# Kernel tuning notes

Measured on AMD Instinct MI355X. Metric: run time of the kernel, lower is better.

## Reference

```python
import jax, jax.numpy as jnp
import numpy as np

B, S, N = 8, 512, 2048   # batch, seq_len (=input_dim=output_dim), num_features (graph nodes)
HID = 512
K = 8                    # k_neighbors


def _construct_adj(x, k):
    """Faithful port of construct_graph: note the original normalizes the
    (1, N) mean-feature vector along dim=1 (whole-vector L2 norm), so the
    'similarity matrix' is actually the outer product v v^T / ||v||^2."""
    Bn, Sn, Nn = x.shape
    fv = x.mean(axis=1)                                  # (B, N)
    nf = fv / jnp.linalg.norm(fv, axis=1, keepdims=True)  # whole-row L2 normalize
    sim = nf[:, :, None] * nf[:, None, :]                # (B, N, N) outer product
    kk = min(k, Nn - 1)
    _, idx = jax.lax.top_k(sim, kk + 1)                  # (B, N, kk+1)
    idx = idx[..., 1:]                                   # drop the single largest (B, N, kk)
    b_ix = jnp.arange(Bn)[:, None, None]
    r_ix = jnp.arange(Nn)[None, :, None]
    adj = jnp.zeros((Bn, Nn, Nn), x.dtype).at[b_ix, r_ix, idx].set(1.0)
    adj = jnp.maximum(adj, jnp.swapaxes(adj, 1, 2))      # symmetrize (adj[idx, i] = 1)
    d = jnp.arange(Nn)
    adj = adj.at[:, d, d].set(1.0)                       # fill_diagonal_(1)
    return adj


def _gc(x, adj, W, b):
    """GraphConvLayer: degree-normalized adjacency bmm after linear."""
    deg = adj.sum(axis=2, keepdims=True)                 # (B, N, 1)
    deg = jnp.where(deg == 0, jnp.ones_like(deg), deg)
    h = x @ W.T + b                                      # (B, N, out)
    return jnp.einsum('bij,bjh->bih', adj / deg, h)


def setup_inputs() -> dict:
    key = jax.random.key(0)
    k0, k1, k2 = jax.random.split(key, 3)
    x = jax.random.normal(k0, (B, S, N), jnp.float32)
    W1 = jax.random.normal(k1, (HID, S), jnp.float32) * 0.02
    b1 = jnp.zeros((HID,), jnp.float32)
    W2 = jax.random.normal(k2, (S, HID), jnp.float32) * 0.02
    b2 = jnp.zeros((S,), jnp.float32)
    return {"x": x, "W1": W1, "b1": b1, "W2": W2, "b2": b2}


def reference(x, W1, b1, W2, b2):
    adj = _construct_adj(x, K)                           # (B, N, N)
    xr = jnp.swapaxes(x, 1, 2)                           # (B, N, S)
    h = jax.nn.relu(_gc(xr, adj, W1, b1))                # (B, N, HID); dropout is eval no-op
    h = _gc(h, adj, W2, b2)                              # (B, N, S)
    return jnp.swapaxes(h, 1, 2)                         # (B, S, N)
```

## Files before the change

kernel.cpp:

```cpp
#include <hip/hip_runtime.h>
#include <hip/hip_bf16.h>
#include <cstdint>

typedef unsigned short u16;
typedef __bf16 bf16x8 __attribute__((ext_vector_type(8)));
typedef float f32x4 __attribute__((ext_vector_type(4)));
typedef float f32x8 __attribute__((ext_vector_type(8)));
typedef unsigned short u16x4 __attribute__((ext_vector_type(4)));
typedef unsigned short u16x8 __attribute__((ext_vector_type(8)));

#define BB 8
#define SS 512
#define NN 2048
#define HH 512
#define MM (BB*NN)

__device__ inline u16 f2b(float f) {
  __hip_bfloat16 h = __float2bfloat16(f);
  return *reinterpret_cast<u16*>(&h);
}
__device__ inline float b2f(u16 u) {
  unsigned x = ((unsigned)u) << 16;
  return __uint_as_float(x);
}
__device__ inline f32x8 b2f8(u16x8 v) {
  f32x8 r;
  #pragma unroll
  for (int k = 0; k < 8; ++k) r[k] = b2f(v[k]);
  return r;
}

#define GLOAD16(g, l) __builtin_amdgcn_global_load_lds( \
    (const __attribute__((address_space(1))) void*)(g), \
    (__attribute__((address_space(3))) void*)(l), 16, 0, 0)

__device__ inline void remap_mn(int bid, int& m0, int& n0) {
  const int xcd = bid & 7, k = bid >> 3;
  m0 = (xcd * 16 + (k >> 2)) * 128;
  n0 = (k & 3) * 128;
}

__global__ __launch_bounds__(256) void k_prep(const float* __restrict__ x, u16* __restrict__ xr,
                       float* __restrict__ fvp,
                       const float* __restrict__ W1, const float* __restrict__ W2,
                       u16* __restrict__ w1b, u16* __restrict__ w2b,
                       float* __restrict__ xs ) {
  const int u = blockIdx.x;
  const int tid = threadIdx.x;
  if (u < 4096) {
    __shared__ float t[64][33];
    __shared__ float ps[8][32];
    const int tx = tid & 31, ty = tid >> 5;
    const int n0 = (u & 63) * 32, st = (u >> 6) & 7, b = u >> 9;
    const int s0 = st * 64;
    float acc = 0.f;
    #pragma unroll
    for (int i = ty; i < 64; i += 8) {
      float w = x[(size_t)b*SS*NN + (size_t)(s0+i)*NN + n0 + tx];
      t[i][tx] = w; acc += w;
    }
    ps[ty][tx] = acc;
    __syncthreads();
    if (ty == 0) {
      float s = 0.f;
      #pragma unroll
      for (int j = 0; j < 8; ++j) s += ps[j][tx];
      fvp[((size_t)(b*8 + st))*NN + n0 + tx] = s;
    }
    const int wtx = tid & 15, wty = tid >> 4;
    #pragma unroll
    for (int j = wty; j < 32; j += 16) {
      ushort4 o;
      o.x = f2b(t[wtx*4+0][j]); o.y = f2b(t[wtx*4+1][j]);
      o.z = f2b(t[wtx*4+2][j]); o.w = f2b(t[wtx*4+3][j]);
      *(ushort4*)(xr + ((size_t)b*NN + n0 + j)*SS + s0 + wtx*4) = o;
    }
    if (u < 96) {
      ((float4*)xs)[u*256 + tid] = make_float4(0.f, 0.f, 0.f, 0.f);
    }
  } else {
    const int b2v = u - 4096;
    const float* Wsrc = (b2v >= 256) ? W2 : W1;
    u16* wb = (b2v >= 256) ? w2b : w1b;
    const int off = (b2v & 255) * 1024;
    float4 v = ((const float4*)(Wsrc + off))[tid];
    ushort4 o; o.x = f2b(v.x); o.y = f2b(v.y); o.z = f2b(v.z); o.w = f2b(v.w);
    *(ushort4*)(wb + off + tid*4) = o;
  }
}

__global__ __launch_bounds__(256) void k_tops(const float* __restrict__ fvp, const u16* __restrict__ xr,
                       int* __restrict__ meta, int* __restrict__ rowfl, float* __restrict__ xs) {
  const int tid = threadIdx.x;
  if (blockIdx.x < BB) {
    const int b = blockIdx.x;
    __shared__ float v[NN];
    __shared__ unsigned long long wk[8];
    __shared__ unsigned long long winner[2];
    __shared__ int sel[18];
    __shared__ int scnt[12];
    __shared__ int ccnt[12];
    const int wv = tid >> 6, ln = tid & 63;

    float lv[8];
    {
      f32x4 a0 = {0,0,0,0}, a1 = {0,0,0,0};
      for (int sb_ = 0; sb_ < 8; ++sb_) {
        const f32x4* p = (const f32x4*)(fvp + ((size_t)(b*8 + sb_))*NN + tid*8);
        a0 += p[0]; a1 += p[1];
      }
      lv[0]=a0[0]; lv[1]=a0[1]; lv[2]=a0[2]; lv[3]=a0[3];
      lv[4]=a1[0]; lv[5]=a1[1]; lv[6]=a1[2]; lv[7]=a1[3];
    }
    #pragma unroll
    for (int j = 0; j < 8; ++j) v[tid*8+j] = lv[j];

    unsigned long long kD[8], kA[8];
    #pragma unroll
    for (int j = 0; j < 8; ++j) {
      unsigned u = __float_as_uint(lv[j]);
      u = (u & 0x80000000u) ? ~u : (u | 0x80000000u);
      unsigned idx = (unsigned)(tid*8 + j);
      kD[j] = ((unsigned long long)u << 32) | (0xFFFFFFFFu - idx);
      kA[j] = ((unsigned long long)(~u) << 32) | (0xFFFFFFFFu - idx);
    }
    unsigned mskD = 0, mskA = 0;
    for (int r = 0; r < 9; ++r) {
      unsigned long long bD = 0ull, bA = 0ull;
      #pragma unroll
      for (int j = 0; j < 8; ++j) {
        if (!((mskD >> j) & 1) && kD[j] > bD) bD = kD[j];
        if (!((mskA >> j) & 1) && kA[j] > bA) bA = kA[j];
      }
      #pragma unroll
      for (int o = 32; o > 0; o >>= 1) {
        unsigned long long oD = __shfl_xor(bD, o, 64);
        unsigned long long oA = __shfl_xor(bA, o, 64);
        if (oD > bD) bD = oD;
        if (oA > bA) bA = oA;
      }
      if (ln == 0) { wk[wv] = bD; wk[4+wv] = bA; }
      __syncthreads();
      if (tid == 0) {
        unsigned long long mD = wk[0], mA = wk[4];
        #pragma unroll
        for (int q = 1; q < 4; ++q) {
          if (wk[q] > mD) mD = wk[q];
          if (wk[4+q] > mA) mA = wk[4+q];
        }
        winner[0] = mD; winner[1] = mA;
        sel[r]   = (int)(0xFFFFFFFFu - (unsigned)mD);
        sel[9+r] = (int)(0xFFFFFFFFu - (unsigned)mA);
      }
      __syncthreads();
      unsigned iD = 0xFFFFFFFFu - (unsigned)winner[0];
      unsigned iA = 0xFFFFFFFFu - (unsigned)winner[1];
      if ((int)(iD >> 3) == tid) mskD |= 1u << (iD & 7);
      if ((int)(iA >> 3) == tid) mskA |= 1u << (iA & 7);
    }

    int cp = 0, cn = 0, cz = 0;
    #pragma unroll
    for (int j = 0; j < 8; ++j) { cp += (lv[j] > 0.f); cn += (lv[j] < 0.f); cz += (lv[j] == 0.f); }
    #pragma unroll
    for (int o = 32; o > 0; o >>= 1) { cp += __shfl_xor(cp, o, 64); cn += __shfl_xor(cn, o, 64); cz += __shfl_xor(cz, o, 64); }
    if (ln == 0) { ccnt[wv] = cp; ccnt[4+wv] = cn; ccnt[8+wv] = cz; }
    __syncthreads();
    if (tid == 0) {
      int CP = 0, CN = 0, CZ = 0;
      #pragma unroll
      for (int q = 0; q < 4; ++q) { CP += ccnt[q]; CN += ccnt[4+q]; CZ += ccnt[8+q]; }
      scnt[0] = CP; scnt[1] = CN; scnt[2] = CZ;
      for (int t2 = 3; t2 < 12; ++t2) scnt[t2] = 0;
      for (int r = 1; r < 9; ++r) {
        float wD = v[sel[r]];   scnt[3] += (wD > 0.f); scnt[4] += (wD < 0.f); scnt[5] += (wD == 0.f);
        float wA = v[sel[9+r]]; scnt[6] += (wA > 0.f); scnt[7] += (wA < 0.f); scnt[8] += (wA == 0.f);
        float wZ = v[r];        scnt[9] += (wZ > 0.f); scnt[10] += (wZ < 0.f); scnt[11] += (wZ == 0.f);
      }
    }
    __syncthreads();
    #pragma unroll
    for (int j = 0; j < 8; ++j) {
      const int i = tid*8 + j;
      float w = lv[j];
      int cls = (w > 0.f) ? 0 : ((w < 0.f) ? 1 : 2);
      int mD = 0, mA = 0;
      #pragma unroll
      for (int r = 1; r < 9; ++r) { mD |= (sel[r] == i); mA |= (sel[9+r] == i); }
      int mZ8 = (i >= 1 && i <= 8);
      rowfl[b*NN + i] = cls | (mD << 2) | (mA << 3) | (mZ8 << 4);
    }
    if (tid < 18) meta[b*32 + tid] = sel[tid];
    if (tid >= 18 && tid < 30) meta[b*32 + tid] = scnt[tid - 18];
    __syncthreads();
    #pragma unroll
    for (int half = 0; half < 2; ++half) {
      const int d = tid + half*256;
      float a[9];
      #pragma unroll
      for (int q = 0; q < 9; ++q) a[q] = 0.f;
      for (int r = 1; r < 9; ++r) {
        int iD = sel[r];   float wD = v[iD]; int cD = (wD>0.f)?0:((wD<0.f)?1:2);
        float vD = b2f(xr[((size_t)b*NN + iD)*512 + d]);
        int iA = sel[9+r]; float wA = v[iA]; int cA = (wA>0.f)?0:((wA<0.f)?1:2);
        float vA = b2f(xr[((size_t)b*NN + iA)*512 + d]);
        float wZ = v[r];   int cZ = (wZ>0.f)?0:((wZ<0.f)?1:2);
        float vZ = b2f(xr[((size_t)b*NN + r)*512 + d]);
        #pragma unroll
        for (int q = 0; q < 3; ++q) {
          a[q]   += (cD == q) ? vD : 0.f;
          a[3+q] += (cA == q) ? vA : 0.f;
          a[6+q] += (cZ == q) ? vZ : 0.f;
        }
      }
      #pragma unroll
      for (int q = 0; q < 9; ++q) xs[((size_t)b*12 + 3 + q)*512 + d] = a[q];
    }
  } else {
    const int u = blockIdx.x - 8, b = u >> 5, c = u & 31, n0 = c*64;
    __shared__ f32x8 red[12][64];
    __shared__ int scls[64];
    if (tid < 64) {
      float s = 0.f;
      for (int sb_ = 0; sb_ < 8; ++sb_) s += fvp[((size_t)(b*8 + sb_))*NN + n0 + tid];
      scls[tid] = (s > 0.f) ? 0 : ((s < 0.f) ? 1 : 2);
    }
    __syncthreads();
    const int fc = tid & 63, rg = tid >> 6;
    f32x8 sp = {0,0,0,0,0,0,0,0}, sn = sp, sz = sp;
    for (int it = 0; it < 16; ++it) {
      const int nr = rg + it*4;
      const int cls = scls[nr];
      f32x8 hf = b2f8(*(const u16x8*)(xr + ((size_t)b*NN + n0 + nr)*512 + fc*8));
      if (cls == 0) sp += hf; else if (cls == 1) sn += hf; else sz += hf;
    }
    red[0*4+rg][fc] = sp; red[1*4+rg][fc] = sn; red[2*4+rg][fc] = sz;
    __syncthreads();
    if (rg == 0) {
      sp = red[0][fc] + red[1][fc] + red[2][fc] + red[3][fc];
      sn = red[4][fc] + red[5][fc] + red[6][fc] + red[7][fc];
      sz = red[8][fc] + red[9][fc] + red[10][fc] + red[11][fc];
      #pragma unroll
      for (int j = 0; j < 8; ++j) {
        atomicAdd(&xs[((size_t)b*12 + 0)*512 + fc*8 + j], sp[j]);
        atomicAdd(&xs[((size_t)b*12 + 1)*512 + fc*8 + j], sn[j]);
        atomicAdd(&xs[((size_t)b*12 + 2)*512 + fc*8 + j], sz[j]);
      }
    }
  }
}

template<int MODE>
__global__ __launch_bounds__(256, 2) void k_gemmf(const u16* __restrict__ A, const u16* __restrict__ Bw,
                       const float* __restrict__ bias, const float* __restrict__ sums,
                       const int* __restrict__ meta, const int* __restrict__ rowfl,
                       void* __restrict__ outp, float* __restrict__ osum) {
  __shared__ __align__(16) char SM[49472];
  u16* As  = (u16*)SM;
  u16* Bs  = (u16*)(SM + 16384);
  u16* xsb = (u16*)(SM + 32768);
  int* cnt = (int*)(SM + 49408);
  const int tid = threadIdx.x;
  const int w = tid >> 6, l = tid & 63;
  const int wm = w >> 1, wn = w & 1;
  int m0, n0; remap_mn(blockIdx.x, m0, n0);
  const int b = m0 >> 11;

  for (int i = tid; i < 12*512; i += 256) {
    const int s = i >> 9, k = i & 511;
    xsb[s*520 + k] = f2b(sums[(size_t)b*12*512 + i]);
  }
  for (int i = tid; i < 4*520; i += 256) xsb[12*520 + i] = 0;
  if (tid < 12) cnt[tid] = meta[b*32 + 18 + tid];

  f32x4 acc[4][4]; f32x4 accV[4];
  #pragma unroll
  for (int i = 0; i < 4; ++i) {
    accV[i] = (f32x4){0.f, 0.f, 0.f, 0.f};
    #pragma unroll
    for (int j = 0; j < 4; ++j) acc[i][j] = (f32x4){0.f, 0.f, 0.f, 0.f};
  }
  const int lr = l & 15;
  const int g4 = l >> 4;
  const int srow8 = l >> 3;
  const int gslot = (l & 7) ^ (srow8 & 7);
  for (int kt = 0; kt < 512; kt += 64) {
    #pragma unroll
    for (int p = 0; p < 4; ++p) {
      const int rbase = w*32 + p*8;
      const int row = rbase + srow8;
      GLOAD16(A  + (size_t)(m0 + row)*512 + kt + gslot*8, As + rbase*64);
      GLOAD16(Bw + (size_t)(n0 + row)*512 + kt + gslot*8, Bs + rbase*64);
    }
    __syncthreads();
    #pragma unroll
    for (int ks = 0; ks < 2; ++ks) {
      bf16x8 af[4], bfr[4];
      #pragma unroll
      for (int i = 0; i < 4; ++i) {
        const int r = wm*64 + i*16 + lr;
        const int lin = (ks*4 + g4) ^ (lr & 7);
        af[i] = *(const bf16x8*)(As + r*64 + lin*8);
      }
      #pragma unroll
      for (int j = 0; j < 4; ++j) {
        const int r = wn*64 + j*16 + lr;
        const int lin = (ks*4 + g4) ^ (lr & 7);
        bfr[j] = *(const bf16x8*)(Bs + r*64 + lin*8);
      }
      #pragma unroll
      for (int i = 0; i < 4; ++i)
        #pragma unroll
        for (int j = 0; j < 4; ++j)
          acc[i][j] = __builtin_amdgcn_mfma_f32_16x16x32_bf16(bfr[j], af[i], acc[i][j], 0, 0, 0);
      if (wm == 0) {
        bf16x8 afx = *(const bf16x8*)(xsb + lr*520 + kt + ks*32 + g4*8);
        #pragma unroll
        for (int j = 0; j < 4; ++j)
          accV[j] = __builtin_amdgcn_mfma_f32_16x16x32_bf16(afx, bfr[j], accV[j], 0, 0, 0);
      }
    }
    __syncthreads();
  }

  float* Vl = (float*)SM;
  if (wm == 0) {
    #pragma unroll
    for (int j = 0; j < 4; ++j) {
      const int c = wn*64 + j*16 + lr;
      const float bv = bias[n0 + c];
      #pragma unroll
      for (int r = 0; r < 4; ++r) {
        const int s = g4*4 + r;
        if (s < 12) Vl[s*128 + c] = accV[j][r] + (float)cnt[s] * bv;
      }
    }
  }
  __syncthreads();

  int fl[4]; float rdg[4]; bool cs[4];
  const float* Vb[4];
  #pragma unroll
  for (int i = 0; i < 4; ++i) {
    const int m = m0 + wm*64 + i*16 + lr;
    const int f = rowfl[m];
    fl[i] = f;
    const int cls = f & 3;
    const int bD = (f >> 2) & 1, bA = (f >> 3) & 1, bZ = (f >> 4) & 1;
    const int rb = 3 + cls*3;
    const int c3c = bD*cnt[0] + bA*cnt[1] + bZ*cnt[2];
    const int c2c = cnt[rb] + cnt[rb+1] + cnt[rb+2] - bD*cnt[rb] - bA*cnt[rb+1] - bZ*cnt[rb+2];
    cs[i] = (cls == 0 && bD) || (cls == 1 && bA) || (cls == 2 && bZ);
    float deg = (float)(c3c + c2c) + (cs[i] ? 0.f : 1.f);
    if (deg < 1.f) deg = 1.f;
    rdg[i] = 1.f / deg;
    Vb[i] = Vl + rb*128;
  }

  if (MODE == 0) {
    u16* G = (u16*)outp;
    float* cbin = (float*)(SM + 8192);
    #pragma unroll
    for (int j = 0; j < 4; ++j) {
      const int dgb = n0 + wn*64 + j*16 + g4*4;
      u16x4 o[4];
      #pragma unroll
      for (int r = 0; r < 4; ++r) {
        const int c = wn*64 + j*16 + g4*4 + r;
        const float bv = bias[dgb + r];
        const float v0 = Vl[c], v1 = Vl[128 + c], v2 = Vl[256 + c];
        float s0 = 0.f, s1 = 0.f, s2 = 0.f;
        #pragma unroll
        for (int i = 0; i < 4; ++i) {
          const int f = fl[i];
          const float t0 = Vb[i][c], t1 = Vb[i][128 + c], t2 = Vb[i][256 + c];
          float c3 = ((f&4)?v0:0.f) + ((f&8)?v1:0.f) + ((f&16)?v2:0.f);
          float c2 = t0 + t1 + t2
                   - ((f&4)?t0:0.f) - ((f&8)?t1:0.f) - ((f&16)?t2:0.f);
          float val = (c3 + c2) * rdg[i];
          if (!cs[i]) val += (acc[i][j][r] + bv) * rdg[i];
          val = fmaxf(val, 0.f);
          o[i][r] = f2b(val);
          const int cls = f & 3;
          s0 += (cls == 0) ? val : 0.f;
          s1 += (cls == 1) ? val : 0.f;
          s2 += (cls == 2) ? val : 0.f;
          if (f & 0x1C) {
            if (f & 4)  atomicAdd(&osum[(size_t)(b*12 + 3 + cls)*512 + dgb + r], val);
            if (f & 8)  atomicAdd(&osum[(size_t)(b*12 + 6 + cls)*512 + dgb + r], val);
            if (f & 16) atomicAdd(&osum[(size_t)(b*12 + 9 + cls)*512 + dgb + r], val);
          }
        }
        #pragma unroll
        for (int o2 = 1; o2 < 16; o2 <<= 1) {
          s0 += __shfl_xor(s0, o2, 64);
          s1 += __shfl_xor(s1, o2, 64);
          s2 += __shfl_xor(s2, o2, 64);
        }
        if (lr == 0) {
          float* cb = cbin + (((wm*2 + wn)*4 + g4)*16 + (j*4 + r))*3;
          cb[0] = s0; cb[1] = s1; cb[2] = s2;
        }
      }
      #pragma unroll
      for (int i = 0; i < 4; ++i)
        *(u16x4*)(G + (size_t)(m0 + wm*64 + i*16 + lr)*512 + dgb) = o[i];
    }
    __syncthreads();
    for (int item = tid; item < 384; item += 256) {
      const int wg = item / 48;
      const int rem = item % 48;
      const int jr = rem / 3, cls = rem % 3;
      const int wnn = wg >> 2, gg = wg & 3;
      const int c = wnn*64 + (jr >> 2)*16 + gg*4 + (jr & 3);
      const float vsum = cbin[(((0*2 + wnn)*4 + gg)*16 + jr)*3 + cls]
                       + cbin[(((1*2 + wnn)*4 + gg)*16 + jr)*3 + cls];
      atomicAdd(&osum[(size_t)(b*12 + cls)*512 + n0 + c], vsum);
    }
  } else {
    float* out = (float*)outp;
    float (*ep)[130] = (float(*)[130])(SM + 8192);
    const int nloc = m0 & 2047;
    for (int j = 0; j < 4; ++j) {
      #pragma unroll
      for (int r = 0; r < 4; ++r) {
        const int c = wn*64 + j*16 + g4*4 + r;
        const float bv = bias[n0 + c];
        const float v0 = Vl[c], v1 = Vl[128 + c], v2 = Vl[256 + c];
        #pragma unroll
        for (int i = 0; i < 4; ++i) {
          const int f = fl[i];
          const float t0 = Vb[i][c], t1 = Vb[i][128 + c], t2 = Vb[i][256 + c];
          float c3 = ((f&4)?v0:0.f) + ((f&8)?v1:0.f) + ((f&16)?v2:0.f);
          float c2 = t0 + t1 + t2
                   - ((f&4)?t0:0.f) - ((f&8)?t1:0.f) - ((f&16)?t2:0.f);
          float val = (c3 + c2) * rdg[i];
          if (!cs[i]) val += (acc[i][j][r] + bv) * rdg[i];
          ep[wn*16 + g4*4 + r][wm*64 + i*16 + lr] = val;
        }
      }
      __syncthreads();
      #pragma unroll
      for (int rr = 0; rr < 8; ++rr) {
        const int q = w*8 + rr;
        const int s = n0 + (q >> 4)*64 + j*16 + (q & 15);
        float2 v2 = *(const float2*)&ep[q][2*l];
        *(float2*)(out + ((size_t)b*SS + s)*NN + nloc + 2*l) = v2;
      }
      __syncthreads();
    }
  }
}

extern "C" void kernel_launch(void* const* d_in, const int* in_sizes, int n_in,
                              void* d_out, int out_size, void* d_ws, size_t ws_size,
                              hipStream_t stream) {
  const float* x  = (const float*)d_in[0];
  const float* W1 = (const float*)d_in[1];
  const float* b1 = (const float*)d_in[2];
  const float* W2 = (const float*)d_in[3];
  const float* b2 = (const float*)d_in[4];
  float* out = (float*)d_out;
  char* ws = (char*)d_ws;

  float* fvp   = (float*)(ws + 0);
  int*   meta  = (int*)  (ws + 1048576);
  int*   rowfl = (int*)  (ws + 1049600);
  float* xs    = (float*)(ws + 1115136);
  float* g1s   = (float*)(ws + 1311744);
  u16*   w1b   = (u16*)  (ws + 1508352);
  u16*   w2b   = (u16*)  (ws + 2032640);
  u16*   g1    = (u16*)  (ws + 2556928);
  u16*   xr    = (u16*)  (ws + 19334144);

  k_prep<<<4608, 256, 0, stream>>>(x, xr, fvp, W1, W2, w1b, w2b, xs);
  k_tops<<<264, 256, 0, stream>>>(fvp, xr, meta, rowfl, xs);
  k_gemmf<0><<<512, 256, 0, stream>>>(xr, w1b, b1, xs, meta, rowfl, (void*)g1, g1s);
  k_gemmf<1><<<512, 256, 0, stream>>>(g1, w2b, b2, g1s, meta, rowfl, (void*)out, nullptr);
}
```

Measured before the change: 92.31 us.

## Double-buffer GEMM shared-memory tiles to overlap global loads with MFMA

```diff
diff --git a/kernel.cpp b/kernel.cpp
--- a/kernel.cpp
+++ b/kernel.cpp
@@ -255,11 +255,9 @@
                        const float* __restrict__ bias, const float* __restrict__ sums,
                        const int* __restrict__ meta, const int* __restrict__ rowfl,
                        void* __restrict__ outp, float* __restrict__ osum) {
-  __shared__ __align__(16) char SM[49472];
-  u16* As  = (u16*)SM;
-  u16* Bs  = (u16*)(SM + 16384);
-  u16* xsb = (u16*)(SM + 32768);
-  int* cnt = (int*)(SM + 49408);
+  __shared__ __align__(16) char SM[78080];
+  u16* xsb = (u16*)(SM + 65536);
+  int* cnt = (int*)(SM + 78016);
   const int tid = threadIdx.x;
   const int w = tid >> 6, l = tid & 63;
   const int wm = w >> 1, wn = w & 1;
@@ -270,7 +268,6 @@
     const int s = i >> 9, k = i & 511;
     xsb[s*520 + k] = f2b(sums[(size_t)b*12*512 + i]);
   }
-  for (int i = tid; i < 4*520; i += 256) xsb[12*520 + i] = 0;
   if (tid < 12) cnt[tid] = meta[b*32 + 18 + tid];
 
   f32x4 acc[4][4]; f32x4 accV[4];
@@ -281,18 +278,41 @@
     for (int j = 0; j < 4; ++j) acc[i][j] = (f32x4){0.f, 0.f, 0.f, 0.f};
   }
   const int lr = l & 15;
+  const int xrow = (lr < 12) ? lr : (lr - 12);
   const int g4 = l >> 4;
   const int srow8 = l >> 3;
   const int gslot = (l & 7) ^ (srow8 & 7);
-  for (int kt = 0; kt < 512; kt += 64) {
-    #pragma unroll
-    for (int p = 0; p < 4; ++p) {
-      const int rbase = w*32 + p*8;
-      const int row = rbase + srow8;
-      GLOAD16(A  + (size_t)(m0 + row)*512 + kt + gslot*8, As + rbase*64);
-      GLOAD16(Bw + (size_t)(n0 + row)*512 + kt + gslot*8, Bs + rbase*64);
-    }
-    __syncthreads();
+
+#define STAGE_T(Ad, Bd, ktq) { \
+    _Pragma("unroll") \
+    for (int p = 0; p < 4; ++p) { \
+      const int rbase = w*32 + p*8; \
+      const int row = rbase + srow8; \
+      GLOAD16(A  + (size_t)(m0 + row)*512 + (ktq) + gslot*8, (Ad) + rbase*64); \
+      GLOAD16(Bw + (size_t)(n0 + row)*512 + (ktq) + gslot*8, (Bd) + rbase*64); \
+    } }
+
+  {
+    u16* As0 = (u16*)SM;
+    u16* Bs0 = (u16*)(SM + 16384);
+    STAGE_T(As0, Bs0, 0);
+  }
+  #pragma unroll
+  for (int t = 0; t < 8; ++t) {
+    u16* Ac = (u16*)(SM + ((t & 1) ? 32768 : 0));
+    u16* Bc = Ac + 8192;
+    u16* An = (u16*)(SM + ((t & 1) ? 0 : 32768));
+    u16* Bn = An + 8192;
+    if (t < 7) {
+      STAGE_T(An, Bn, (t+1)*64);
+      asm volatile("s_waitcnt vmcnt(8)" ::: "memory");
+    } else {
+      asm volatile("s_waitcnt vmcnt(0)" ::: "memory");
+    }
+    __builtin_amdgcn_sched_barrier(0);
+    __builtin_amdgcn_s_barrier();
+    __builtin_amdgcn_sched_barrier(0);
+    const int kt = t * 64;
     #pragma unroll
     for (int ks = 0; ks < 2; ++ks) {
       bf16x8 af[4], bfr[4];
@@ -300,13 +320,13 @@
       for (int i = 0; i < 4; ++i) {
         const int r = wm*64 + i*16 + lr;
         const int lin = (ks*4 + g4) ^ (lr & 7);
-        af[i] = *(const bf16x8*)(As + r*64 + lin*8);
+        af[i] = *(const bf16x8*)(Ac + r*64 + lin*8);
       }
       #pragma unroll
       for (int j = 0; j < 4; ++j) {
         const int r = wn*64 + j*16 + lr;
         const int lin = (ks*4 + g4) ^ (lr & 7);
-        bfr[j] = *(const bf16x8*)(Bs + r*64 + lin*8);
+        bfr[j] = *(const bf16x8*)(Bc + r*64 + lin*8);
       }
       #pragma unroll
       for (int i = 0; i < 4; ++i)
@@ -314,14 +334,17 @@
         for (int j = 0; j < 4; ++j)
           acc[i][j] = __builtin_amdgcn_mfma_f32_16x16x32_bf16(bfr[j], af[i], acc[i][j], 0, 0, 0);
       if (wm == 0) {
-        bf16x8 afx = *(const bf16x8*)(xsb + lr*520 + kt + ks*32 + g4*8);
+        bf16x8 afx = *(const bf16x8*)(xsb + xrow*520 + kt + ks*32 + g4*8);
         #pragma unroll
         for (int j = 0; j < 4; ++j)
           accV[j] = __builtin_amdgcn_mfma_f32_16x16x32_bf16(afx, bfr[j], accV[j], 0, 0, 0);
       }
     }
-    __syncthreads();
-  }
+    __builtin_amdgcn_sched_barrier(0);
+    __builtin_amdgcn_s_barrier();
+    __builtin_amdgcn_sched_barrier(0);
+  }
+#undef STAGE_T
 
   float* Vl = (float*)SM;
   if (wm == 0) {
```

After: 92.21 us. Within noise of the previous version (-0.1%).
